# Performance work log

Measured on AMD Instinct MI355X. Metric: run time of the kernel, lower is better.

Reference implementation:

```python
import jax, jax.numpy as jnp
import numpy as np

N, E, B = 16384, 262144, 64
F, FE, T, FOUT = 32, 16, 8, 4      # node dim, edge dim, towers, per-tower out (T*FOUT == F)
L, H, A, S = 3, 128, 4, 3          # pna layers, mlp hidden, n_aggregators, n_scalers
EPS = 1e-5


def setup_inputs() -> dict:
    key = jax.random.key(0)
    ks = jax.random.split(key, 16)
    s = 0.1
    return {
        'x': jax.random.randint(ks[0], (N,), 0, F),
        'edge_index': jax.random.randint(ks[1], (2, E), 0, N),
        'edge_attr': jax.random.randint(ks[2], (E,), 0, FE),
        'batch': jnp.sort(jax.random.randint(ks[3], (N,), 0, B)),
        'node_emb': jax.random.normal(ks[4], (F, F)) * s,
        'edge_emb': jax.random.normal(ks[5], (FE, FE)) * s,
        'Wee': jax.random.normal(ks[6], (L, FE, F)) * s,   # per-layer edge encoder
        'bee': jnp.zeros((L, F)),
        'Wpre': jax.random.normal(ks[7], (L, T, 3 * F, F)) * s,   # per-tower pre-MLP
        'bpre': jnp.zeros((L, T, F)),
        'Wpost': jax.random.normal(ks[8], (L, T, (A * S + 1) * F, FOUT)) * s,  # per-tower post-MLP
        'bpost': jnp.zeros((L, T, FOUT)),
        'Wlin': jax.random.normal(ks[9], (L, F, F)) * s,   # tower-mixing linear
        'blin': jnp.zeros((L, F)),
        'bng': jnp.ones((L, F)),
        'bnb': jnp.zeros((L, F)),
        'Wm0': jax.random.normal(ks[10], (F, H)) * s,
        'bm0': jnp.zeros((H,)),
        'Wmh': jax.random.normal(ks[11], (2, H, H)) * s,
        'bmh': jnp.zeros((2, H)),
        'bnmg': jnp.ones((3, H)),
        'bnmb': jnp.zeros((3, H)),
        'Wf': jax.random.normal(ks[12], (H, 1)) * s,
        'bf': jnp.zeros((1,)),
    }


def _bn(x, g, b):
    # BatchNorm forward with batch statistics (training-mode math)
    mu = x.mean(0)
    var = x.var(0)
    return (x - mu) * jax.lax.rsqrt(var + EPS) * g + b


def reference(x, edge_index, edge_attr, batch, node_emb, edge_emb, Wee, bee,
              Wpre, bpre, Wpost, bpost, Wlin, blin, bng, bnb,
              Wm0, bm0, Wmh, bmh, bnmg, bnmb, Wf, bf):
    src, dst = edge_index[0], edge_index[1]
    h = node_emb[x]                  # [N,F]
    ea = edge_emb[edge_attr]         # [E,FE]
    # in-degree of target nodes; avg log-degree stands in for the train-set deg histogram
    deg = jax.ops.segment_sum(jnp.ones((E,), h.dtype), dst, num_segments=N)
    avg_log = jnp.mean(jnp.log(deg + 1.0))
    dc = jnp.maximum(deg, 1.0)
    amp = (jnp.log(dc + 1.0) / avg_log)[:, None, None]       # amplification scaler
    att = (avg_log / jnp.log(dc + 1.0))[:, None, None]       # attenuation scaler
    has = (deg > 0)[:, None, None]
    inv_cnt = (1.0 / dc)[:, None, None]
    for l in range(L):
        e = ea @ Wee[l] + bee[l]                              # [E,F]
        m = jnp.concatenate([h[dst], h[src], e], axis=-1)     # [E,3F]  (x_i, x_j, edge)
        msg = jnp.einsum('ec,tcf->etf', m, Wpre[l]) + bpre[l] # [E,T,F]
        ssum = jax.ops.segment_sum(msg, dst, num_segments=N)
        mean = ssum * inv_cnt
        meansq = jax.ops.segment_sum(msg * msg, dst, num_segments=N) * inv_cnt
        std = jnp.sqrt(jax.nn.relu(meansq - mean * mean) + EPS)
        mn = jnp.where(has, jax.ops.segment_min(msg, dst, num_segments=N), 0.0)
        mx = jnp.where(has, jax.ops.segment_max(msg, dst, num_segments=N), 0.0)
        agg = jnp.concatenate([mean, mn, mx, std], axis=-1)   # [N,T,A*F]
        out = jnp.concatenate([agg, agg * amp, agg * att], axis=-1)  # [N,T,A*S*F]
        out = jnp.concatenate(
            [jnp.broadcast_to(h[:, None, :], (h.shape[0], T, F)), out], axis=-1)
        out = jnp.einsum('ntc,tcf->ntf', out, Wpost[l]) + bpost[l]   # [N,T,FOUT]
        out = out.reshape(-1, T * FOUT) @ Wlin[l] + blin[l]          # [N,F]
        h = jax.nn.relu(_bn(out, bng[l], bnb[l]))
    g = jax.ops.segment_sum(h, batch, num_segments=B)                # global_add_pool [B,F]
    g = jax.nn.relu(_bn(g @ Wm0 + bm0, bnmg[0], bnmb[0]))
    for i in range(2):
        g = jax.nn.relu(_bn(g @ Wmh[i] + bmh[i], bnmg[i + 1], bnmb[i + 1]))
    logits = g @ Wf + bf                                             # [B,1]
    return jax.nn.sigmoid(logits), logits
```

## Files before the change

### kernel.cpp

```cpp
#include <hip/hip_runtime.h>
#include <hip/hip_bf16.h>
#include <math.h>

#define NN 16384
#define NE 262144
#define NB 64
#define FD 32
#define NT 8
#define NL 3
#define NH 128
#define EPSV 1e-5f

typedef unsigned short u16;
typedef unsigned int u32;
typedef long long i64;

static __device__ __forceinline__ float us2f(u16 u){
  union { u32 i; float f; } z; z.i = ((u32)u) << 16; return z.f;
}
static __device__ __forceinline__ u16 f2us(float v){
  __hip_bfloat16 b = __float2bfloat16(v);
  return *(u16*)&b;
}

__global__ void k_diag(float* out, float v){
  int i = threadIdx.x;
  if (i < 128) out[i] = v;
}

__global__ __launch_bounds__(256) void k_detect(const u16* __restrict__ ne, int* __restrict__ flags){
  __shared__ float red[256];
  const int tid = threadIdx.x;
  float m = 0.f;
  for (int i=tid; i<1024; i+=256) m = fmaxf(m, fabsf(us2f(ne[i])));
  red[tid]=m; __syncthreads();
  for (int off=128; off>0; off>>=1){ if (tid<off) red[tid]=fmaxf(red[tid],red[tid+off]); __syncthreads(); }
  if (tid==0) flags[0] = (red[0] > 100.f) ? 1 : 0;
}

__global__ __launch_bounds__(256) void k_det_i64(const int* __restrict__ ei_raw, int* __restrict__ flags){
  __shared__ int red[256];
  const int tid = threadIdx.x;
  int i = blockIdx.x*256 + tid;
  int c = (i < NE && ei_raw[2*i+1] == 0) ? 1 : 0;
  red[tid]=c; __syncthreads();
  for (int off=128; off>0; off>>=1){ if (tid<off) red[tid]+=red[tid+off]; __syncthreads(); }
  if (tid==0) atomicAdd(&flags[4], red[0]);
}

struct IJobs { const void* src[4]; int* dst[4]; int cnt[4]; };
__global__ __launch_bounds__(256) void k_cvt_int(IJobs jb, const int* __restrict__ flags,
                                                 int* __restrict__ deg, int total){
  int i = blockIdx.x*256 + threadIdx.x;
  if (i >= total) return;
  const int m = (flags[4] > NE/4) ? 1 : 0;
  int a = 0, off = i;
  while (off >= jb.cnt[a]){ off -= jb.cnt[a]; a++; }
  int v = m ? (int)((const i64*)jb.src[a])[off] : ((const int*)jb.src[a])[off];
  jb.dst[a][off] = v;
  if (a == 1 && off >= NE && v >= 0 && v < NN) atomicAdd(&deg[v], 1);
}

struct Jobs { const void* src[20]; float* dst[20]; int cnt[20]; };
__global__ __launch_bounds__(256) void k_cvt(Jobs jb, const int* __restrict__ flags, int total){
  int i = blockIdx.x*256 + threadIdx.x;
  if (i >= total) return;
  const int m = flags[0];
  int a = 0, off = i;
  while (off >= jb.cnt[a]){ off -= jb.cnt[a]; a++; }
  float v = m ? ((const float*)jb.src[a])[off]
              : us2f(((const u16*)jb.src[a])[off]);
  jb.dst[a][off] = v;
}

__global__ __launch_bounds__(256) void k_scan(const int* __restrict__ deg, int* __restrict__ offs,
                                              double* __restrict__ lsum){
  __shared__ int part[257];
  __shared__ double red[256];
  const int tid = threadIdx.x;
  int s = 0; double ls = 0.0;
  for (int i=0;i<64;i++){ int d = deg[tid*64+i]; s += d; ls += log((double)d + 1.0); }
  part[tid+1] = s; red[tid] = ls;
  __syncthreads();
  if (tid==0){ part[0]=0; for (int i=1;i<=256;i++) part[i]+=part[i-1]; }
  for (int off=128; off>0; off>>=1){ if (tid<off) red[tid]+=red[tid+off]; __syncthreads(); }
  if (tid==0) *lsum = red[0] / (double)NN;
  __syncthreads();
  int run = part[tid];
  for (int i=0;i<64;i++){ offs[tid*64+i]=run; run+=deg[tid*64+i]; }
  if (tid==255) offs[NN]=run;
}

__global__ void k_fill(const int* __restrict__ src, const int* __restrict__ dst,
                       const int* __restrict__ ea_in, const int* __restrict__ offs,
                       int* __restrict__ cursor, int* __restrict__ esrc, int* __restrict__ eatt){
  int e = blockIdx.x*256 + threadIdx.x;
  if (e < NE){
    int d = dst[e];
    int pslot = atomicAdd(&cursor[d], 1);
    int idx = offs[d] + pslot;
    esrc[idx] = src[e];
    eatt[idx] = ea_in[e];
  }
}

__global__ void k_nodeprep(const int* __restrict__ deg, const double* __restrict__ lsum,
                           const int* __restrict__ batch,
                           float* __restrict__ amp, float* __restrict__ attn, float* __restrict__ invc,
                           int* __restrict__ bstart){
  int n = blockIdx.x*256 + threadIdx.x;
  if (n >= NN) return;
  float avg = (float)(*lsum);
  int d = deg[n]; int dc = d > 0 ? d : 1;
  float la = logf((float)dc + 1.0f);
  amp[n] = la/avg; attn[n] = avg/la; invc[n] = 1.0f/(float)dc;
  int b = batch[n];
  int prev = (n==0) ? -1 : batch[n-1];
  for (int v=prev+1; v<=b; v++) bstart[v]=n;
  if (n==NN-1) for (int v=b+1; v<=NB; v++) bstart[v]=NN;
}

__global__ __launch_bounds__(256) void k_etab3(const float* __restrict__ ee, const float* __restrict__ Wee,
                      const float* __restrict__ bee, const float* __restrict__ Wpre,
                      float* __restrict__ etab, int l){
  __shared__ float el[16*FD];
  const int tid = threadIdx.x;
  for (int i=tid; i<16*FD; i+=256){
    int a = i>>5, f2 = i&31;
    float acc = bee[l*FD + f2];
    for (int c2=0; c2<16; c2++)
      acc = fmaf(ee[a*16+c2], Wee[(l*16+c2)*FD+f2], acc);
    el[i] = acc;
  }
  __syncthreads();
  int i = blockIdx.x*256 + tid;
  int a = i>>8, dd = i&255, t = dd>>5, f = dd&31;
  float acc = 0.f;
  for (int f2=0; f2<FD; f2++)
    acc = fmaf(el[a*FD+f2], Wpre[((l*NT+t)*96 + 64 + f2)*FD + f], acc);
  etab[i] = acc;
}

__global__ __launch_bounds__(256) void k_pre(
    const float* __restrict__ z, const double* __restrict__ st,
    const float* __restrict__ bng, const float* __restrict__ bnb,
    const int* __restrict__ x, const float* __restrict__ emb,
    const float* __restrict__ Wpre, const float* __restrict__ bpre,
    float* __restrict__ h, float* __restrict__ nbase, u16* __restrict__ psrcH, int l)
{
  __shared__ float hl[64*FD];
  __shared__ float scl[FD], shl[FD];
  const int tid = threadIdx.x;
  const int n0 = blockIdx.x*64;
  if (l == 0){
    for (int i=tid; i<64*FD; i+=256)
      hl[i] = emb[x[n0+(i>>5)]*FD + (i&31)];
  } else {
    if (tid < FD){
      const double* stL = st + (l-1)*64;
      double mu = stL[tid] * (1.0/(double)NN);
      double var = stL[32+tid] * (1.0/(double)NN) - mu*mu;
      float sc = bng[(l-1)*FD+tid]*rsqrtf(fmaxf((float)var,0.f)+EPSV);
      scl[tid]=sc; shl[tid]=bnb[(l-1)*FD+tid]-(float)mu*sc;
    }
    __syncthreads();
    for (int i=tid; i<64*FD; i+=256){
      int f = i&31;
      hl[i] = fmaxf(z[n0*FD+i]*scl[f]+shl[f], 0.f);
    }
  }
  __syncthreads();
  for (int i=tid; i<64*FD; i+=256) h[n0*FD+i] = hl[i];
  const int t = tid>>5, f = tid&31;
  float wd[32], ws[32];
  #pragma unroll
  for (int c=0;c<FD;c++){
    wd[c] = Wpre[((l*NT+t)*96 + c)*FD + f];
    ws[c] = Wpre[((l*NT+t)*96 + 32 + c)*FD + f];
  }
  const float bb = bpre[(l*NT+t)*FD + f];
  for (int nn=0; nn<64; nn++){
    float ad=bb, as=0.f;
    #pragma unroll
    for (int c=0;c<FD;c++){ float hv=hl[nn*FD+c]; ad=fmaf(hv,wd[c],ad); as=fmaf(hv,ws[c],as); }
    const int n = n0+nn;
    nbase[(size_t)n*256+tid]=ad;
    psrcH[(size_t)n*256+tid]=f2us(as);
  }
}

__global__ __launch_bounds__(1024) void k_agg(
    const float* __restrict__ nbase, const u16* __restrict__ psrcH,
    const float* __restrict__ etab,
    const int* __restrict__ esrc, const int* __restrict__ eatt, const int* __restrict__ offs,
    const float* __restrict__ h, const float* __restrict__ amp,
    const float* __restrict__ attn, const float* __restrict__ invc,
    const float* __restrict__ Wpost, const float* __restrict__ bpost,
    const float* __restrict__ Wlin, const float* __restrict__ blin,
    float* __restrict__ z, double* __restrict__ st, int l)
{
  __shared__ u16 wp[13312];
  __shared__ float wl[1024];
  __shared__ float etl[4096];
  __shared__ float bpo[32], bli[32];
  __shared__ float s1[16*32], s2[16*32];
  const int tid = threadIdx.x;
  const float* WpL = Wpost + (size_t)l*13312;
  for (int i=tid;i<13312;i+=1024) wp[i] = (u16)(__float_as_uint(WpL[i])>>16);
  if (tid < 1024) wl[tid] = Wlin[l*1024+tid];
  for (int i=tid;i<4096;i+=1024) etl[i] = etab[i];
  if (tid<32){ bpo[tid]=bpost[l*32+tid]; bli[tid]=blin[l*32+tid]; }
  __syncthreads();
  const int wid = tid>>6, lane = tid&63;
  const int t = lane>>3, q = lane&7;
  const int n = blockIdx.x*16 + wid;
  const int o0 = offs[n], o1 = offs[n+1];
  float bs[4]; *(float4*)bs = *(const float4*)(nbase + (size_t)n*256 + lane*4);
  float sum[4]={0,0,0,0}, sq[4]={0,0,0,0}, mn[4], mx[4];
  #pragma unroll
  for (int k=0;k<4;k++){ mn[k]=__builtin_inff(); mx[k]=-__builtin_inff(); }
  int j = o0;
  for (; j+3 < o1; j+=4){
    const int s0=esrc[j],   s1_=esrc[j+1], s2_=esrc[j+2], s3=esrc[j+3];
    const int a0=eatt[j],   a1=eatt[j+1], a2=eatt[j+2], a3=eatt[j+3];
    ushort4 p0 = *(const ushort4*)(psrcH + (size_t)s0*256 + lane*4);
    ushort4 p1 = *(const ushort4*)(psrcH + (size_t)s1_*256 + lane*4);
    ushort4 p2 = *(const ushort4*)(psrcH + (size_t)s2_*256 + lane*4);
    ushort4 p3 = *(const ushort4*)(psrcH + (size_t)s3*256 + lane*4);
    float4 e0 = *(const float4*)(etl + a0*256 + lane*4);
    float4 e1 = *(const float4*)(etl + a1*256 + lane*4);
    float4 e2 = *(const float4*)(etl + a2*256 + lane*4);
    float4 e3 = *(const float4*)(etl + a3*256 + lane*4);
    const u16* pp0=(const u16*)&p0; const float* ee0=(const float*)&e0;
    const u16* pp1=(const u16*)&p1; const float* ee1=(const float*)&e1;
    const u16* pp2=(const u16*)&p2; const float* ee2=(const float*)&e2;
    const u16* pp3=(const u16*)&p3; const float* ee3=(const float*)&e3;
    #pragma unroll
    for (int k=0;k<4;k++){
      float v0 = bs[k] + us2f(pp0[k]) + ee0[k];
      float v1 = bs[k] + us2f(pp1[k]) + ee1[k];
      float v2 = bs[k] + us2f(pp2[k]) + ee2[k];
      float v3 = bs[k] + us2f(pp3[k]) + ee3[k];
      sum[k] += (v0+v1)+(v2+v3);
      sq[k] = fmaf(v0,v0,sq[k]); sq[k] = fmaf(v1,v1,sq[k]);
      sq[k] = fmaf(v2,v2,sq[k]); sq[k] = fmaf(v3,v3,sq[k]);
      mn[k] = fminf(mn[k], fminf(fminf(v0,v1), fminf(v2,v3)));
      mx[k] = fmaxf(mx[k], fmaxf(fmaxf(v0,v1), fmaxf(v2,v3)));
    }
  }
  for (; j < o1; j++){
    const int s = esrc[j];
    const int a = eatt[j];
    ushort4 pv4 = *(const ushort4*)(psrcH + (size_t)s*256 + lane*4);
    float4 ev4 = *(const float4*)(etl + a*256 + lane*4);
    const u16* pv=(const u16*)&pv4; const float* ev=(const float*)&ev4;
    #pragma unroll
    for (int k=0;k<4;k++){
      float v = bs[k] + us2f(pv[k]) + ev[k];
      sum[k]+=v; sq[k]=fmaf(v,v,sq[k]); mn[k]=fminf(mn[k],v); mx[k]=fmaxf(mx[k],v);
    }
  }
  const int dg = o1-o0;
  const float ic = invc[n];
  float aggv[4][4];
  #pragma unroll
  for (int k=0;k<4;k++){
    float mean = sum[k]*ic;
    float ms = sq[k]*ic;
    float var = fmaxf(ms - mean*mean, 0.f);
    aggv[0][k]=mean;
    aggv[1][k]=(dg>0)?mn[k]:0.f;
    aggv[2][k]=(dg>0)?mx[k]:0.f;
    aggv[3][k]=sqrtf(var+EPSV);
  }
  const float av = amp[n], at_ = attn[n];
  float acc[4]={0,0,0,0};
  float hv[4]; *(float4*)hv = *(const float4*)(h + n*FD + q*4);
  #pragma unroll
  for (int k=0;k<4;k++){
    int c = q*4+k;
    #pragma unroll
    for (int jj=0;jj<4;jj++)
      acc[jj] = fmaf(hv[k], us2f(wp[(t*416+c)*4+jj]), acc[jj]);
  }
  #pragma unroll
  for (int g=0; g<4; g++){
    #pragma unroll
    for (int k=0;k<4;k++){
      float a_ = aggv[g][k];
      int rb = 32 + g*32 + q*4 + k;
      #pragma unroll
      for (int jj=0;jj<4;jj++){
        float w = us2f(wp[(t*416+rb)*4+jj])
                + av*us2f(wp[(t*416+rb+128)*4+jj])
                + at_*us2f(wp[(t*416+rb+256)*4+jj]);
        acc[jj] = fmaf(a_, w, acc[jj]);
      }
    }
  }
  #pragma unroll
  for (int jj=0;jj<4;jj++){
    acc[jj] += __shfl_xor(acc[jj], 1);
    acc[jj] += __shfl_xor(acc[jj], 2);
    acc[jj] += __shfl_xor(acc[jj], 4);
    acc[jj] += bpo[t*4+jj];
  }
  float zv = 0.f;
  #pragma unroll
  for (int dp=0; dp<32; dp++){
    float v = __shfl(acc[dp&3], (dp>>2)*8);
    zv = fmaf(v, wl[dp*32 + (lane&31)], zv);
  }
  float zfin = zv + bli[lane&31];
  if (lane < 32){
    z[n*FD + lane] = zfin;
    s1[wid*32+lane] = zfin;
    s2[wid*32+lane] = zfin*zfin;
  }
  __syncthreads();
  if (tid < 32){
    float a1=0.f, a2=0.f;
    #pragma unroll
    for (int w=0; w<16; w++){ a1 += s1[w*32+tid]; a2 += s2[w*32+tid]; }
    atomicAdd(&st[l*64+tid],    (double)a1);
    atomicAdd(&st[l*64+32+tid], (double)a2);
  }
}

__global__ __launch_bounds__(256) void k_pool2(const float* __restrict__ z, const double* __restrict__ st,
                                               const float* __restrict__ bng, const float* __restrict__ bnb,
                                               const int* __restrict__ bstart, float* __restrict__ g){
  __shared__ float acc[8][FD];
  __shared__ float scl[FD], shl[FD];
  const int b = blockIdx.x;
  const int tid = threadIdx.x;
  const int f = tid&31, rg = tid>>5;
  if (tid < FD){
    const double* stL = st + (NL-1)*64;
    double mu = stL[tid] * (1.0/(double)NN);
    double var = stL[32+tid] * (1.0/(double)NN) - mu*mu;
    float sc = bng[(NL-1)*FD+tid]*rsqrtf(fmaxf((float)var,0.f)+EPSV);
    scl[tid]=sc; shl[tid]=bnb[(NL-1)*FD+tid]-(float)mu*sc;
  }
  __syncthreads();
  const int lo = bstart[b], hi = bstart[b+1];
  float s = 0.f;
  for (int n=lo+rg; n<hi; n+=8) s += fmaxf(z[n*FD+f]*scl[f]+shl[f], 0.f);
  acc[rg][f] = s; __syncthreads();
  if (rg == 0){
    float t = 0.f;
    for (int r=0;r<8;r++) t += acc[r][f];
    g[b*FD+f] = t;
  }
}

__global__ __launch_bounds__(256) void k_hgemm(const float* __restrict__ in, const float* __restrict__ W,
                                               const float* __restrict__ bias, float* __restrict__ outp,
                                               int IN){
  int o = blockIdx.x*256 + threadIdx.x;
  int b = o>>7, hh = o&127;
  float acc = bias[hh];
  for (int c=0;c<IN;c++) acc = fmaf(in[b*IN+c], W[c*NH+hh], acc);
  outp[o] = acc;
}

__global__ __launch_bounds__(512) void k_hbn(float* __restrict__ buf,
                                             const float* __restrict__ gvec, const float* __restrict__ bvec){
  __shared__ float scf[NH], shf[NH];
  const int tid = threadIdx.x;
  const int f = tid>>2, part = tid&3;
  double s1=0.0, s2=0.0;
  for (int b=part*16; b<part*16+16; b++){
    double v = (double)buf[b*NH+f]; s1+=v; s2+=v*v;
  }
  s1 += __shfl_xor(s1, 1); s2 += __shfl_xor(s2, 1);
  s1 += __shfl_xor(s1, 2); s2 += __shfl_xor(s2, 2);
  if (part==0){
    double mu = s1/(double)NB;
    double var = s2/(double)NB - mu*mu;
    float varf = fmaxf((float)var, 0.f);
    float sc = gvec[f]*rsqrtf(varf+EPSV);
    scf[f]=sc; shf[f]=bvec[f]-(float)mu*sc;
  }
  __syncthreads();
  for (int i=tid; i<NB*NH; i+=512){
    int hh = i&127;
    buf[i] = fmaxf(buf[i]*scf[hh]+shf[hh], 0.f);
  }
}

__global__ __launch_bounds__(64) void k_hfin(const float* __restrict__ buf, const float* __restrict__ Wf,
                                             const float* __restrict__ bfv, float* __restrict__ out){
  int b = threadIdx.x;
  float acc = bfv[0];
  for (int c=0;c<NH;c++) acc = fmaf(buf[b*NH+c], Wf[c], acc);
  out[NB+b] = acc;
  out[b]    = 1.f/(1.f+expf(-acc));
}

extern "C" void kernel_launch(void* const* d_in, const int* in_sizes, int n_in,
                              void* d_out, int out_size, void* d_ws, size_t ws_size,
                              hipStream_t stream)
{
  float* out = (float*)d_out;

  static const int EXP_SZ[24] = {16384, 524288, 262144, 16384, 1024, 256, 1536, 96,
                                 73728, 768, 39936, 96, 3072, 96, 96, 96,
                                 4096, 128, 32768, 256, 384, 384, 128, 1};
  int bad = -1;
  if (n_in != 24) bad = 24;
  else for (int i=0;i<24;i++){ if (in_sizes[i] != EXP_SZ[i]){ bad = i; break; } }
  if (bad >= 0){
    k_diag<<<1, 128, 0, stream>>>(out, 512.0f + 8.0f*(float)bad);
    return;
  }

  char* p = (char*)d_ws;
  auto carve = [&](size_t bytes)->char*{ char* r = p; p += (bytes + 255) & ~(size_t)255; return r; };
  int*    flags = (int*)carve(256);
  double* st1   = (double*)carve(3*64*8);
  int*    deg   = (int*)carve((size_t)NN*4);
  int*    cursor= (int*)carve((size_t)NN*4);
  size_t  zspan = (size_t)(((char*)cursor + ((NN*4+255)&~(size_t)255)) - (char*)flags);
  int*    offs  = (int*)carve((size_t)(NN+1)*4);
  int*    esrc  = (int*)carve((size_t)NE*4);
  int*    eatt  = (int*)carve((size_t)NE*4);
  int*    bstart= (int*)carve((size_t)(NB+1)*4);
  float*  h     = (float*)carve((size_t)NN*FD*4);
  float*  z     = (float*)carve((size_t)NN*FD*4);
  float*  nbase = (float*)carve((size_t)NN*256*4);
  u16*    psrcH = (u16*)carve((size_t)NN*256*2);
  float*  etab  = (float*)carve(4096*4);
  float*  amp   = (float*)carve((size_t)NN*4);
  float*  attn  = (float*)carve((size_t)NN*4);
  float*  invc  = (float*)carve((size_t)NN*4);
  double* lsum  = (double*)carve(8);
  float*  gp    = (float*)carve((size_t)NB*FD*4);
  float*  t0    = (float*)carve((size_t)NB*NH*4);
  float*  t1    = (float*)carve((size_t)NB*NH*4);
  float*  t2    = (float*)carve((size_t)NB*NH*4);
  int*    cx    = (int*)carve((size_t)NN*4);
  int*    cei   = (int*)carve((size_t)2*NE*4);
  int*    cea   = (int*)carve((size_t)NE*4);
  int*    cbatch= (int*)carve((size_t)NN*4);

  Jobs jb;
  float* wptr[24];
  int total = 0;
  {
    float* cur = (float*)carve(700*1024);
    for (int i=4; i<24; i++){
      jb.src[i-4] = d_in[i];
      jb.dst[i-4] = cur;
      jb.cnt[i-4] = in_sizes[i];
      wptr[i] = cur;
      cur += in_sizes[i];
      total += in_sizes[i];
    }
  }
  const size_t need = (size_t)(p - (char*)d_ws);
  if (ws_size < need){
    k_diag<<<1, 128, 0, stream>>>(out, -2000.0f - (float)(ws_size >> 20));
    return;
  }

  IJobs ij;
  ij.src[0]=d_in[0]; ij.dst[0]=cx;     ij.cnt[0]=NN;
  ij.src[1]=d_in[1]; ij.dst[1]=cei;    ij.cnt[1]=2*NE;
  ij.src[2]=d_in[2]; ij.dst[2]=cea;    ij.cnt[2]=NE;
  ij.src[3]=d_in[3]; ij.dst[3]=cbatch; ij.cnt[3]=NN;
  const int itotal = NN + 2*NE + NE + NN;

  const float* ne_f   = wptr[4];
  const float* ee_f   = wptr[5];
  const float* Wee_f  = wptr[6];
  const float* bee_f  = wptr[7];
  const float* Wpre_f = wptr[8];
  const float* bpre_f = wptr[9];
  const float* Wpost_f= wptr[10];
  const float* bpost_f= wptr[11];
  const float* Wlin_f = wptr[12];
  const float* blin_f = wptr[13];
  const float* bng_f  = wptr[14];
  const float* bnb_f  = wptr[15];
  const float* Wm0_f  = wptr[16];
  const float* bm0_f  = wptr[17];
  const float* Wmh_f  = wptr[18];
  const float* bmh_f  = wptr[19];
  const float* bnmg_f = wptr[20];
  const float* bnmb_f = wptr[21];
  const float* Wf_f   = wptr[22];
  const float* bf_f   = wptr[23];

  hipMemsetAsync(flags, 0, zspan, stream);

  k_detect<<<1, 256, 0, stream>>>((const u16*)d_in[4], flags);
  k_det_i64<<<NE/256, 256, 0, stream>>>((const int*)d_in[1], flags);
  k_cvt_int<<<(itotal+255)/256, 256, 0, stream>>>(ij, flags, deg, itotal);
  k_cvt<<<(total+255)/256, 256, 0, stream>>>(jb, flags, total);

  k_scan<<<1, 256, 0, stream>>>(deg, offs, lsum);
  k_fill<<<NE/256, 256, 0, stream>>>(cei, cei+NE, cea, offs, cursor, esrc, eatt);
  k_nodeprep<<<NN/256, 256, 0, stream>>>(deg, lsum, cbatch, amp, attn, invc, bstart);

  for (int l=0; l<NL; l++){
    k_etab3<<<16, 256, 0, stream>>>(ee_f, Wee_f, bee_f, Wpre_f, etab, l);
    k_pre<<<NN/64, 256, 0, stream>>>(z, st1, bng_f, bnb_f, cx, ne_f, Wpre_f, bpre_f,
                                     h, nbase, psrcH, l);
    k_agg<<<NN/16, 1024, 0, stream>>>(nbase, psrcH, etab, esrc, eatt, offs, h, amp, attn, invc,
                                      Wpost_f, bpost_f, Wlin_f, blin_f, z, st1, l);
  }

  k_pool2<<<NB, 256, 0, stream>>>(z, st1, bng_f, bnb_f, bstart, gp);
  k_hgemm<<<32, 256, 0, stream>>>(gp, Wm0_f, bm0_f, t0, FD);
  k_hbn<<<1, 512, 0, stream>>>(t0, bnmg_f, bnmb_f);
  k_hgemm<<<32, 256, 0, stream>>>(t0, Wmh_f, bmh_f, t1, NH);
  k_hbn<<<1, 512, 0, stream>>>(t1, bnmg_f+NH, bnmb_f+NH);
  k_hgemm<<<32, 256, 0, stream>>>(t1, Wmh_f+NH*NH, bmh_f+NH, t2, NH);
  k_hbn<<<1, 512, 0, stream>>>(t2, bnmg_f+2*NH, bnmb_f+2*NH);
  k_hfin<<<1, 64, 0, stream>>>(t2, Wf_f, bf_f, out);
}
```

Baseline: 408.7 us.

## Sort nodes by degree for aggregation, store nbase in bf16, merge detect kernels

Builds a degree histogram and counting-sort permutation so each aggregation block of 16 wavefronts processes nodes of similar in-degree. The goal is less load imbalance inside a block. The per-node base pre-activation is stored as bf16 instead of fp32, halving that buffer's write and read traffic at some precision cost. The two input-detection kernels are merged into one launch. Output indexing still uses the node id, so results land correctly, but node ordering within a block loses locality of the z writes.

```diff
diff --git a/kernel.cpp b/kernel.cpp
--- a/kernel.cpp
+++ b/kernel.cpp
@@ -28,19 +28,19 @@
   if (i < 128) out[i] = v;
 }
 
-__global__ __launch_bounds__(256) void k_detect(const u16* __restrict__ ne, int* __restrict__ flags){
-  __shared__ float red[256];
-  const int tid = threadIdx.x;
-  float m = 0.f;
-  for (int i=tid; i<1024; i+=256) m = fmaxf(m, fabsf(us2f(ne[i])));
-  red[tid]=m; __syncthreads();
-  for (int off=128; off>0; off>>=1){ if (tid<off) red[tid]=fmaxf(red[tid],red[tid+off]); __syncthreads(); }
-  if (tid==0) flags[0] = (red[0] > 100.f) ? 1 : 0;
-}
-
-__global__ __launch_bounds__(256) void k_det_i64(const int* __restrict__ ei_raw, int* __restrict__ flags){
+__global__ __launch_bounds__(256) void k_det(const u16* __restrict__ ne, const int* __restrict__ ei_raw,
+                                             int* __restrict__ flags){
   __shared__ int red[256];
   const int tid = threadIdx.x;
+  if (blockIdx.x == 0){
+    __shared__ float redf[256];
+    float m = 0.f;
+    for (int i=tid; i<1024; i+=256) m = fmaxf(m, fabsf(us2f(ne[i])));
+    redf[tid]=m; __syncthreads();
+    for (int off=128; off>0; off>>=1){ if (tid<off) redf[tid]=fmaxf(redf[tid],redf[tid+off]); __syncthreads(); }
+    if (tid==0) flags[0] = (redf[0] > 100.f) ? 1 : 0;
+    __syncthreads();
+  }
   int i = blockIdx.x*256 + tid;
   int c = (i < NE && ei_raw[2*i+1] == 0) ? 1 : 0;
   red[tid]=c; __syncthreads();
@@ -107,17 +107,34 @@
 __global__ void k_nodeprep(const int* __restrict__ deg, const double* __restrict__ lsum,
                            const int* __restrict__ batch,
                            float* __restrict__ amp, float* __restrict__ attn, float* __restrict__ invc,
-                           int* __restrict__ bstart){
+                           int* __restrict__ bstart, int* __restrict__ hist){
   int n = blockIdx.x*256 + threadIdx.x;
   if (n >= NN) return;
   float avg = (float)(*lsum);
   int d = deg[n]; int dc = d > 0 ? d : 1;
   float la = logf((float)dc + 1.0f);
   amp[n] = la/avg; attn[n] = avg/la; invc[n] = 1.0f/(float)dc;
+  atomicAdd(&hist[d < 127 ? d : 127], 1);
   int b = batch[n];
   int prev = (n==0) ? -1 : batch[n-1];
   for (int v=prev+1; v<=b; v++) bstart[v]=n;
   if (n==NN-1) for (int v=b+1; v<=NB; v++) bstart[v]=NN;
+}
+
+__global__ void k_bucket(const int* __restrict__ hist, int* __restrict__ boff){
+  if (threadIdx.x==0){
+    int run=0;
+    for (int i=0;i<128;i++){ boff[i]=run; run+=hist[i]; }
+  }
+}
+
+__global__ void k_perm(const int* __restrict__ deg, const int* __restrict__ boff,
+                       int* __restrict__ bcur, int* __restrict__ perm){
+  int n = blockIdx.x*256 + threadIdx.x;
+  if (n >= NN) return;
+  int d = deg[n]; int b = d < 127 ? d : 127;
+  int pos = atomicAdd(&bcur[b], 1);
+  perm[boff[b]+pos] = n;
 }
 
 __global__ __launch_bounds__(256) void k_etab3(const float* __restrict__ ee, const float* __restrict__ Wee,
@@ -146,7 +163,7 @@
     const float* __restrict__ bng, const float* __restrict__ bnb,
     const int* __restrict__ x, const float* __restrict__ emb,
     const float* __restrict__ Wpre, const float* __restrict__ bpre,
-    float* __restrict__ h, float* __restrict__ nbase, u16* __restrict__ psrcH, int l)
+    float* __restrict__ h, u16* __restrict__ nbaseH, u16* __restrict__ psrcH, int l)
 {
   __shared__ float hl[64*FD];
   __shared__ float scl[FD], shl[FD];
@@ -184,14 +201,14 @@
     #pragma unroll
     for (int c=0;c<FD;c++){ float hv=hl[nn*FD+c]; ad=fmaf(hv,wd[c],ad); as=fmaf(hv,ws[c],as); }
     const int n = n0+nn;
-    nbase[(size_t)n*256+tid]=ad;
+    nbaseH[(size_t)n*256+tid]=f2us(ad);
     psrcH[(size_t)n*256+tid]=f2us(as);
   }
 }
 
 __global__ __launch_bounds__(1024) void k_agg(
-    const float* __restrict__ nbase, const u16* __restrict__ psrcH,
-    const float* __restrict__ etab,
+    const u16* __restrict__ nbaseH, const u16* __restrict__ psrcH,
+    const float* __restrict__ etab, const int* __restrict__ perm,
     const int* __restrict__ esrc, const int* __restrict__ eatt, const int* __restrict__ offs,
     const float* __restrict__ h, const float* __restrict__ amp,
     const float* __restrict__ attn, const float* __restrict__ invc,
@@ -213,9 +230,15 @@
   __syncthreads();
   const int wid = tid>>6, lane = tid&63;
   const int t = lane>>3, q = lane&7;
-  const int n = blockIdx.x*16 + wid;
+  const int n = perm[blockIdx.x*16 + wid];
   const int o0 = offs[n], o1 = offs[n+1];
-  float bs[4]; *(float4*)bs = *(const float4*)(nbase + (size_t)n*256 + lane*4);
+  float bs[4];
+  {
+    ushort4 b4 = *(const ushort4*)(nbaseH + (size_t)n*256 + lane*4);
+    const u16* bb=(const u16*)&b4;
+    #pragma unroll
+    for (int k=0;k<4;k++) bs[k] = us2f(bb[k]);
+  }
   float sum[4]={0,0,0,0}, sq[4]={0,0,0,0}, mn[4], mx[4];
   #pragma unroll
   for (int k=0;k<4;k++){ mn[k]=__builtin_inff(); mx[k]=-__builtin_inff(); }
@@ -419,16 +442,20 @@
   auto carve = [&](size_t bytes)->char*{ char* r = p; p += (bytes + 255) & ~(size_t)255; return r; };
   int*    flags = (int*)carve(256);
   double* st1   = (double*)carve(3*64*8);
+  int*    hist  = (int*)carve(128*4);
+  int*    bcur  = (int*)carve(128*4);
   int*    deg   = (int*)carve((size_t)NN*4);
   int*    cursor= (int*)carve((size_t)NN*4);
   size_t  zspan = (size_t)(((char*)cursor + ((NN*4+255)&~(size_t)255)) - (char*)flags);
+  int*    boff  = (int*)carve(128*4);
+  int*    perm  = (int*)carve((size_t)NN*4);
   int*    offs  = (int*)carve((size_t)(NN+1)*4);
   int*    esrc  = (int*)carve((size_t)NE*4);
   int*    eatt  = (int*)carve((size_t)NE*4);
   int*    bstart= (int*)carve((size_t)(NB+1)*4);
   float*  h     = (float*)carve((size_t)NN*FD*4);
   float*  z     = (float*)carve((size_t)NN*FD*4);
-  float*  nbase = (float*)carve((size_t)NN*256*4);
+  u16*    nbaseH= (u16*)carve((size_t)NN*256*2);
   u16*    psrcH = (u16*)carve((size_t)NN*256*2);
   float*  etab  = (float*)carve(4096*4);
   float*  amp   = (float*)carve((size_t)NN*4);
@@ -494,20 +521,21 @@
 
   hipMemsetAsync(flags, 0, zspan, stream);
 
-  k_detect<<<1, 256, 0, stream>>>((const u16*)d_in[4], flags);
-  k_det_i64<<<NE/256, 256, 0, stream>>>((const int*)d_in[1], flags);
+  k_det<<<NE/256, 256, 0, stream>>>((const u16*)d_in[4], (const int*)d_in[1], flags);
   k_cvt_int<<<(itotal+255)/256, 256, 0, stream>>>(ij, flags, deg, itotal);
   k_cvt<<<(total+255)/256, 256, 0, stream>>>(jb, flags, total);
 
   k_scan<<<1, 256, 0, stream>>>(deg, offs, lsum);
   k_fill<<<NE/256, 256, 0, stream>>>(cei, cei+NE, cea, offs, cursor, esrc, eatt);
-  k_nodeprep<<<NN/256, 256, 0, stream>>>(deg, lsum, cbatch, amp, attn, invc, bstart);
+  k_nodeprep<<<NN/256, 256, 0, stream>>>(deg, lsum, cbatch, amp, attn, invc, bstart, hist);
+  k_bucket<<<1, 64, 0, stream>>>(hist, boff);
+  k_perm<<<NN/256, 256, 0, stream>>>(deg, boff, bcur, perm);
 
   for (int l=0; l<NL; l++){
     k_etab3<<<16, 256, 0, stream>>>(ee_f, Wee_f, bee_f, Wpre_f, etab, l);
     k_pre<<<NN/64, 256, 0, stream>>>(z, st1, bng_f, bnb_f, cx, ne_f, Wpre_f, bpre_f,
-                                     h, nbase, psrcH, l);
-    k_agg<<<NN/16, 1024, 0, stream>>>(nbase, psrcH, etab, esrc, eatt, offs, h, amp, attn, invc,
+                                     h, nbaseH, psrcH, l);
+    k_agg<<<NN/16, 1024, 0, stream>>>(nbaseH, psrcH, etab, perm, esrc, eatt, offs, h, amp, attn, invc,
                                       Wpost_f, bpost_f, Wlin_f, blin_f, z, st1, l);
   }
 
```

Result: slower. 499.4 us (+22.2%).
